# Optimization experiments

Hardware: AMD Instinct MI355X
Metric: run time of the kernel (lower is better)

The kernel has to match this reference:

```python
import jax, jax.numpy as jnp
import numpy as np

TOP_K = 10  # hard-coded k=10 in the original tf.nn.top_k call


def setup_inputs() -> dict:
    key = jax.random.key(0)
    k1, k2 = jax.random.split(key)
    x = jax.random.normal(k1, (32768, 128), dtype=jnp.float32)
    cluster_centers = jax.random.normal(k2, (512, 128), dtype=jnp.float32)
    return {"x": x, "cluster_centers": cluster_centers}


def reference(x, cluster_centers):
    # (mathematically identical to tf.norm(x[:, None, :] - centers, axis=-1)
    #  without materializing the [N, K, D] difference tensor).
    x2 = jnp.sum(x * x, axis=-1, keepdims=True)            # [N, 1]
    c2 = jnp.sum(cluster_centers * cluster_centers, -1)    # [K]
    d2 = x2 - 2.0 * (x @ cluster_centers.T) + c2           # [N, K]
    distances = jnp.sqrt(jnp.maximum(d2, 0.0))
    # top-k smallest distances -> cluster indices (values in [0, K))
    _, indices = jax.lax.top_k(-distances, TOP_K)          # [N, 10] int32
    # Faithful to the original: gather POINTS x at these cluster indices
    closest_points = x[indices]                            # [N, 10, D]
    return closest_points.reshape(1, -1, x.shape[-1])      # [1, N*10, D]
```

## Files before the change

kernel.cpp:

```cpp
#include <hip/hip_runtime.h>
#include <stdint.h>

#define NPTS 32768
#define NCEN 512
#define DIM  128
#define TOPK 10

#define BM 128
#define BN 128
#define KSTEP 32
#define LDT 132

__global__ __launch_bounds__(256) void np_rownorm(const float* __restrict__ src,
                                                  float* __restrict__ dst, int nrows) {
  const int t = threadIdx.x;
  const int lane = t & 63;
  const int wv = t >> 6;
  const int g = lane >> 3;
  const int j = lane & 7;
  const int row = blockIdx.x * 32 + wv * 8 + g;
  if (row >= nrows) return;
  const float* p = src + (size_t)row * DIM;

  float v = p[j];
  float r = __fmul_rn(v, v);
#pragma unroll
  for (int b = 1; b < 16; ++b) {
    v = p[8 * b + j];
    r = __fadd_rn(r, __fmul_rn(v, v));
  }
  r = __fadd_rn(r, __shfl_xor(r, 1, 64));
  r = __fadd_rn(r, __shfl_xor(r, 2, 64));
  r = __fadd_rn(r, __shfl_xor(r, 4, 64));
  if (j == 0) dst[row] = r;
}

__global__ __launch_bounds__(256, 4) void dist_kernel(const float* __restrict__ x,
                                                      const float* __restrict__ cen,
                                                      const float* __restrict__ x2,
                                                      const float* __restrict__ c2,
                                                      float* __restrict__ dist) {
  __shared__ float xT[KSTEP][LDT];
  __shared__ float cT[KSTEP][LDT];

  const int t  = threadIdx.x;
  const int pb = blockIdx.y * BM;
  const int cb = blockIdx.x * BN;

  const int srow = t & 127;
  const int kh   = (t >> 7) * 16;

  const int wid  = t >> 6;
  const int lane = t & 63;
  const int wr = wid >> 1, wc = wid & 1;
  const int r = lane & 7, c = lane >> 3;
  const int px = wr * 64 + 4 * r;
  const int cx = wc * 64 + 4 * c;

  float acc[8][8];
#pragma unroll
  for (int i = 0; i < 8; ++i)
#pragma unroll
    for (int j = 0; j < 8; ++j) acc[i][j] = 0.f;

  for (int s = 0; s < DIM / KSTEP; ++s) {
    if (s) __syncthreads();
    {
      const float4* srcx = (const float4*)&x[(size_t)(pb + srow) * DIM + s * KSTEP + kh];
      const float4* srcc = (const float4*)&cen[(size_t)(cb + srow) * DIM + s * KSTEP + kh];
#pragma unroll
      for (int i = 0; i < 4; ++i) {
        float4 v = srcx[i];
        int k = kh + i * 4;
        xT[k + 0][srow] = v.x; xT[k + 1][srow] = v.y; xT[k + 2][srow] = v.z; xT[k + 3][srow] = v.w;
      }
#pragma unroll
      for (int i = 0; i < 4; ++i) {
        float4 v = srcc[i];
        int k = kh + i * 4;
        cT[k + 0][srow] = v.x; cT[k + 1][srow] = v.y; cT[k + 2][srow] = v.z; cT[k + 3][srow] = v.w;
      }
    }
    __syncthreads();

#pragma unroll 4
    for (int kk = 0; kk < KSTEP; ++kk) {
      float4 xa  = *(const float4*)&xT[kk][px];
      float4 xb  = *(const float4*)&xT[kk][px + 32];
      float4 ca  = *(const float4*)&cT[kk][cx];
      float4 cbv = *(const float4*)&cT[kk][cx + 32];
      float xv[8] = {xa.x, xa.y, xa.z, xa.w, xb.x, xb.y, xb.z, xb.w};
      float cv[8] = {ca.x, ca.y, ca.z, ca.w, cbv.x, cbv.y, cbv.z, cbv.w};
#pragma unroll
      for (int i = 0; i < 8; ++i)
#pragma unroll
        for (int j = 0; j < 8; ++j)
          acc[i][j] = __fmaf_rn(xv[i], cv[j], acc[i][j]);
    }
  }

#pragma unroll
  for (int i = 0; i < 8; ++i) {
    const int pt = px + (i & 3) + (i >> 2) * 32;
    const int p  = pb + pt;
    const float xx = x2[p];
#pragma unroll
    for (int jq = 0; jq < 2; ++jq) {
      const int cg = cb + cx + jq * 32;
      float4 cc = *(const float4*)&c2[cg];
      float t0 = __fmaf_rn(-2.f, acc[i][jq * 4 + 0], xx);
      float t1 = __fmaf_rn(-2.f, acc[i][jq * 4 + 1], xx);
      float t2 = __fmaf_rn(-2.f, acc[i][jq * 4 + 2], xx);
      float t3 = __fmaf_rn(-2.f, acc[i][jq * 4 + 3], xx);
      float4 o;
      o.x = sqrtf(fmaxf(__fadd_rn(t0, cc.x), 0.f));
      o.y = sqrtf(fmaxf(__fadd_rn(t1, cc.y), 0.f));
      o.z = sqrtf(fmaxf(__fadd_rn(t2, cc.z), 0.f));
      o.w = sqrtf(fmaxf(__fadd_rn(t3, cc.w), 0.f));
      *(float4*)&dist[(size_t)p * NCEN + cg] = o;
    }
  }
}

__global__ __launch_bounds__(256) void topk_gather_kernel(const float* __restrict__ dist,
                                                          const float* __restrict__ x,
                                                          float* __restrict__ out) {
  const int p    = blockIdx.x * 4 + (threadIdx.x >> 6);
  const int lane = threadIdx.x & 63;

  const float4* dp = (const float4*)(dist + (size_t)p * NCEN);
  float4 va = dp[lane];
  float4 vb = dp[lane + 64];

  unsigned long long key[8];
  {
    const unsigned ca = 4u * lane, cb = 256u + 4u * lane;
    key[0] = ((unsigned long long)__float_as_uint(va.x) << 32) | (ca + 0);
    key[1] = ((unsigned long long)__float_as_uint(va.y) << 32) | (ca + 1);
    key[2] = ((unsigned long long)__float_as_uint(va.z) << 32) | (ca + 2);
    key[3] = ((unsigned long long)__float_as_uint(va.w) << 32) | (ca + 3);
    key[4] = ((unsigned long long)__float_as_uint(vb.x) << 32) | (cb + 0);
    key[5] = ((unsigned long long)__float_as_uint(vb.y) << 32) | (cb + 1);
    key[6] = ((unsigned long long)__float_as_uint(vb.z) << 32) | (cb + 2);
    key[7] = ((unsigned long long)__float_as_uint(vb.w) << 32) | (cb + 3);
  }

  float* op = out + (size_t)p * TOPK * DIM;

#pragma unroll
  for (int t = 0; t < TOPK; ++t) {
    unsigned long long m = key[0];
#pragma unroll
    for (int s = 1; s < 8; ++s) m = (key[s] < m) ? key[s] : m;
#pragma unroll
    for (int off = 32; off > 0; off >>= 1) {
      unsigned long long o = __shfl_xor(m, off, 64);
      m = (o < m) ? o : m;
    }
#pragma unroll
    for (int s = 0; s < 8; ++s)
      if (key[s] == m) key[s] = ~0ull;

    const int idx = (int)(m & 0x1ffull);
    float2 v = *(const float2*)&x[(size_t)idx * DIM + 2 * lane];
    *(float2*)&op[(size_t)t * DIM + 2 * lane] = v;
  }
}

extern "C" void kernel_launch(void* const* d_in, const int* in_sizes, int n_in,
                              void* d_out, int out_size, void* d_ws, size_t ws_size,
                              hipStream_t stream) {
  const float* x   = (const float*)d_in[0];
  const float* cen = (const float*)d_in[1];
  float* out = (float*)d_out;

  float* c2   = (float*)d_ws;
  float* x2   = (float*)((char*)d_ws + 4096);
  float* dist = (float*)((char*)d_ws + 4096 + 131072);

  np_rownorm<<<NCEN / 32, 256, 0, stream>>>(cen, c2, NCEN);
  np_rownorm<<<NPTS / 32, 256, 0, stream>>>(x, x2, NPTS);
  dist_kernel<<<dim3(NCEN / BN, NPTS / BM), 256, 0, stream>>>(x, cen, x2, c2, dist);
  topk_gather_kernel<<<NPTS / 4, 256, 0, stream>>>(dist, x, out);
}
```

Baseline: 123.6 us.

## Fuse distance GEMM, top-k selection and gather into one kernel

Each 1024-thread block now computes distances from 128 points to all 512 centers and performs a per-wave top-10 followed by a shared-memory merge. It then gathers the selected rows directly into the output. This removes the global write and re-read of the full distance matrix and one kernel launch. In exchange, occupancy is lower with large shared memory and big blocks, and each block runs its compute, selection and gather phases serially.

Result: slower. 135.7 us (+9.8%).

```diff
diff --git a/kernel.cpp b/kernel.cpp
--- a/kernel.cpp
+++ b/kernel.cpp
@@ -1,15 +1,19 @@
 #include <hip/hip_runtime.h>
 #include <stdint.h>
+
+typedef unsigned long long u64;
 
 #define NPTS 32768
 #define NCEN 512
 #define DIM  128
 #define TOPK 10
 
-#define BM 128
-#define BN 128
 #define KSTEP 32
-#define LDT 132
+#define LDX 132
+#define LDC 516
+#define KPAD 81
+
+#define SMEM_BYTES 88064
 
 __global__ __launch_bounds__(256) void np_rownorm(const float* __restrict__ src,
                                                   float* __restrict__ dst, int nrows) {
@@ -35,24 +39,23 @@
   if (j == 0) dst[row] = r;
 }
 
-__global__ __launch_bounds__(256, 4) void dist_kernel(const float* __restrict__ x,
-                                                      const float* __restrict__ cen,
-                                                      const float* __restrict__ x2,
-                                                      const float* __restrict__ c2,
-                                                      float* __restrict__ dist) {
-  __shared__ float xT[KSTEP][LDT];
-  __shared__ float cT[KSTEP][LDT];
+__global__ __launch_bounds__(1024, 4) void fused_kernel(const float* __restrict__ x,
+                                                        const float* __restrict__ cen,
+                                                        const float* __restrict__ x2,
+                                                        const float* __restrict__ c2,
+                                                        float* __restrict__ out) {
+  __shared__ __align__(16) char smem[SMEM_BYTES];
+  float* xT = (float*)smem;
+  float* cT = (float*)(smem + (size_t)KSTEP * LDX * 4);
+  u64*  keysL   = (u64*)smem;
+  unsigned* mergedL = (unsigned*)(smem + (size_t)128 * KPAD * 8);
 
   const int t  = threadIdx.x;
-  const int pb = blockIdx.y * BM;
-  const int cb = blockIdx.x * BN;
-
-  const int srow = t & 127;
-  const int kh   = (t >> 7) * 16;
+  const int pb = blockIdx.x * 128;
 
   const int wid  = t >> 6;
   const int lane = t & 63;
-  const int wr = wid >> 1, wc = wid & 1;
+  const int wr = wid >> 3, wc = wid & 7;
   const int r = lane & 7, c = lane >> 3;
   const int px = wr * 64 + 4 * r;
   const int cx = wc * 64 + 4 * c;
@@ -63,34 +66,41 @@
 #pragma unroll
     for (int j = 0; j < 8; ++j) acc[i][j] = 0.f;
 
+  const int xrow = t & 127, xkh = ((t >> 7) & 1) * 16;
+  const int crow = t & 511, ckh = (t >> 9) * 16;
+
   for (int s = 0; s < DIM / KSTEP; ++s) {
     if (s) __syncthreads();
-    {
-      const float4* srcx = (const float4*)&x[(size_t)(pb + srow) * DIM + s * KSTEP + kh];
-      const float4* srcc = (const float4*)&cen[(size_t)(cb + srow) * DIM + s * KSTEP + kh];
+    if (t < 256) {
+      const float4* srcx = (const float4*)&x[(size_t)(pb + xrow) * DIM + s * KSTEP + xkh];
 #pragma unroll
       for (int i = 0; i < 4; ++i) {
         float4 v = srcx[i];
-        int k = kh + i * 4;
-        xT[k + 0][srow] = v.x; xT[k + 1][srow] = v.y; xT[k + 2][srow] = v.z; xT[k + 3][srow] = v.w;
+        int k = xkh + i * 4;
+        xT[(k + 0) * LDX + xrow] = v.x; xT[(k + 1) * LDX + xrow] = v.y;
+        xT[(k + 2) * LDX + xrow] = v.z; xT[(k + 3) * LDX + xrow] = v.w;
       }
+    }
+    {
+      const float4* srcc = (const float4*)&cen[(size_t)crow * DIM + s * KSTEP + ckh];
 #pragma unroll
       for (int i = 0; i < 4; ++i) {
         float4 v = srcc[i];
-        int k = kh + i * 4;
-        cT[k + 0][srow] = v.x; cT[k + 1][srow] = v.y; cT[k + 2][srow] = v.z; cT[k + 3][srow] = v.w;
+        int k = ckh + i * 4;
+        cT[(k + 0) * LDC + crow] = v.x; cT[(k + 1) * LDC + crow] = v.y;
+        cT[(k + 2) * LDC + crow] = v.z; cT[(k + 3) * LDC + crow] = v.w;
       }
     }
     __syncthreads();
 
 #pragma unroll 4
     for (int kk = 0; kk < KSTEP; ++kk) {
-      float4 xa  = *(const float4*)&xT[kk][px];
-      float4 xb  = *(const float4*)&xT[kk][px + 32];
-      float4 ca  = *(const float4*)&cT[kk][cx];
-      float4 cbv = *(const float4*)&cT[kk][cx + 32];
+      float4 xa  = *(const float4*)&xT[kk * LDX + px];
+      float4 xb  = *(const float4*)&xT[kk * LDX + px + 32];
+      float4 ca  = *(const float4*)&cT[kk * LDC + cx];
+      float4 cb2 = *(const float4*)&cT[kk * LDC + cx + 32];
       float xv[8] = {xa.x, xa.y, xa.z, xa.w, xb.x, xb.y, xb.z, xb.w};
-      float cv[8] = {ca.x, ca.y, ca.z, ca.w, cbv.x, cbv.y, cbv.z, cbv.w};
+      float cv[8] = {ca.x, ca.y, ca.z, ca.w, cb2.x, cb2.y, cb2.z, cb2.w};
 #pragma unroll
       for (int i = 0; i < 8; ++i)
 #pragma unroll
@@ -98,72 +108,78 @@
           acc[i][j] = __fmaf_rn(xv[i], cv[j], acc[i][j]);
     }
   }
+  __syncthreads();
 
+  const float4 cc0 = *(const float4*)&c2[cx];
+  const float4 cc1 = *(const float4*)&c2[cx + 32];
 #pragma unroll
   for (int i = 0; i < 8; ++i) {
     const int pt = px + (i & 3) + (i >> 2) * 32;
-    const int p  = pb + pt;
-    const float xx = x2[p];
+    const float xx = x2[pb + pt];
+    u64 key[8];
 #pragma unroll
     for (int jq = 0; jq < 2; ++jq) {
-      const int cg = cb + cx + jq * 32;
-      float4 cc = *(const float4*)&c2[cg];
+      const float4 cc = jq ? cc1 : cc0;
       float t0 = __fmaf_rn(-2.f, acc[i][jq * 4 + 0], xx);
       float t1 = __fmaf_rn(-2.f, acc[i][jq * 4 + 1], xx);
       float t2 = __fmaf_rn(-2.f, acc[i][jq * 4 + 2], xx);
       float t3 = __fmaf_rn(-2.f, acc[i][jq * 4 + 3], xx);
-      float4 o;
-      o.x = sqrtf(fmaxf(__fadd_rn(t0, cc.x), 0.f));
-      o.y = sqrtf(fmaxf(__fadd_rn(t1, cc.y), 0.f));
-      o.z = sqrtf(fmaxf(__fadd_rn(t2, cc.z), 0.f));
-      o.w = sqrtf(fmaxf(__fadd_rn(t3, cc.w), 0.f));
-      *(float4*)&dist[(size_t)p * NCEN + cg] = o;
+      float d0 = sqrtf(fmaxf(__fadd_rn(t0, cc.x), 0.f));
+      float d1 = sqrtf(fmaxf(__fadd_rn(t1, cc.y), 0.f));
+      float d2 = sqrtf(fmaxf(__fadd_rn(t2, cc.z), 0.f));
+      float d3 = sqrtf(fmaxf(__fadd_rn(t3, cc.w), 0.f));
+      const unsigned cbase = (unsigned)(cx + 32 * jq);
+      key[jq * 4 + 0] = ((u64)__float_as_uint(d0) << 32) | (cbase + 0);
+      key[jq * 4 + 1] = ((u64)__float_as_uint(d1) << 32) | (cbase + 1);
+      key[jq * 4 + 2] = ((u64)__float_as_uint(d2) << 32) | (cbase + 2);
+      key[jq * 4 + 3] = ((u64)__float_as_uint(d3) << 32) | (cbase + 3);
+    }
+#pragma unroll
+    for (int tt = 0; tt < TOPK; ++tt) {
+      u64 m = key[0];
+#pragma unroll
+      for (int s2 = 1; s2 < 8; ++s2) m = (key[s2] < m) ? key[s2] : m;
+      u64 o;
+      o = __shfl_xor(m, 8, 64);  m = (o < m) ? o : m;
+      o = __shfl_xor(m, 16, 64); m = (o < m) ? o : m;
+      o = __shfl_xor(m, 32, 64); m = (o < m) ? o : m;
+      if (c == 0) keysL[(size_t)pt * KPAD + wc * 10 + tt] = m;
+#pragma unroll
+      for (int s2 = 0; s2 < 8; ++s2)
+        if (key[s2] == m) key[s2] = ~0ull;
     }
   }
-}
+  __syncthreads();
 
-__global__ __launch_bounds__(256) void topk_gather_kernel(const float* __restrict__ dist,
-                                                          const float* __restrict__ x,
-                                                          float* __restrict__ out) {
-  const int p    = blockIdx.x * 4 + (threadIdx.x >> 6);
-  const int lane = threadIdx.x & 63;
+  {
+    const int g  = lane >> 3;
+    const int cs = lane & 7;
+    const int mp = wid * 8 + g;
+    int ptr = 0;
+#pragma unroll
+    for (int tt = 0; tt < TOPK; ++tt) {
+      u64 head = (ptr < 10) ? keysL[(size_t)mp * KPAD + cs * 10 + ptr] : ~0ull;
+      u64 m = head;
+      u64 o;
+      o = __shfl_xor(m, 1, 64); m = (o < m) ? o : m;
+      o = __shfl_xor(m, 2, 64); m = (o < m) ? o : m;
+      o = __shfl_xor(m, 4, 64); m = (o < m) ? o : m;
+      if (head == m) ptr++;
+      if (cs == 0) mergedL[mp * 10 + tt] = (unsigned)(m & 0x1ffu);
+    }
+  }
+  __syncthreads();
 
-  const float4* dp = (const float4*)(dist + (size_t)p * NCEN);
-  float4 va = dp[lane];
-  float4 vb = dp[lane + 64];
-
-  unsigned long long key[8];
   {
-    const unsigned ca = 4u * lane, cb = 256u + 4u * lane;
-    key[0] = ((unsigned long long)__float_as_uint(va.x) << 32) | (ca + 0);
-    key[1] = ((unsigned long long)__float_as_uint(va.y) << 32) | (ca + 1);
-    key[2] = ((unsigned long long)__float_as_uint(va.z) << 32) | (ca + 2);
-    key[3] = ((unsigned long long)__float_as_uint(va.w) << 32) | (ca + 3);
-    key[4] = ((unsigned long long)__float_as_uint(vb.x) << 32) | (cb + 0);
-    key[5] = ((unsigned long long)__float_as_uint(vb.y) << 32) | (cb + 1);
-    key[6] = ((unsigned long long)__float_as_uint(vb.z) << 32) | (cb + 2);
-    key[7] = ((unsigned long long)__float_as_uint(vb.w) << 32) | (cb + 3);
-  }
-
-  float* op = out + (size_t)p * TOPK * DIM;
-
-#pragma unroll
-  for (int t = 0; t < TOPK; ++t) {
-    unsigned long long m = key[0];
-#pragma unroll
-    for (int s = 1; s < 8; ++s) m = (key[s] < m) ? key[s] : m;
-#pragma unroll
-    for (int off = 32; off > 0; off >>= 1) {
-      unsigned long long o = __shfl_xor(m, off, 64);
-      m = (o < m) ? o : m;
+#pragma unroll 4
+    for (int rr = 0; rr < 80; ++rr) {
+      const int row = wid * 80 + rr;
+      const int p  = row / 10;
+      const int tt = row - p * 10;
+      const int idx = mergedL[p * 10 + tt];
+      const float2 v = *(const float2*)&x[(size_t)idx * DIM + 2 * lane];
+      *(float2*)&out[(((size_t)(pb + p)) * TOPK + tt) * DIM + 2 * lane] = v;
     }
-#pragma unroll
-    for (int s = 0; s < 8; ++s)
-      if (key[s] == m) key[s] = ~0ull;
-
-    const int idx = (int)(m & 0x1ffull);
-    float2 v = *(const float2*)&x[(size_t)idx * DIM + 2 * lane];
-    *(float2*)&op[(size_t)t * DIM + 2 * lane] = v;
   }
 }
 
@@ -174,12 +190,10 @@
   const float* cen = (const float*)d_in[1];
   float* out = (float*)d_out;
 
-  float* c2   = (float*)d_ws;
-  float* x2   = (float*)((char*)d_ws + 4096);
-  float* dist = (float*)((char*)d_ws + 4096 + 131072);
+  float* c2 = (float*)d_ws;
+  float* x2 = (float*)((char*)d_ws + 4096);
 
   np_rownorm<<<NCEN / 32, 256, 0, stream>>>(cen, c2, NCEN);
   np_rownorm<<<NPTS / 32, 256, 0, stream>>>(x, x2, NPTS);
-  dist_kernel<<<dim3(NCEN / BN, NPTS / BM), 256, 0, stream>>>(x, cen, x2, c2, dist);
-  topk_gather_kernel<<<NPTS / 4, 256, 0, stream>>>(dist, x, out);
+  fused_kernel<<<NPTS / 128, 1024, 0, stream>>>(x, cen, x2, c2, out);
 }
```
